# Optimization experiments

Measured on AMD Instinct MI355X. Metric: run time of the kernel, lower is better.

The kernel has to match this reference:

```python
import jax, jax.numpy as jnp
import numpy as np

N_NODES = 100000
N_EDGES = 600000
IN_DIM = 128
OUT_DIM = 64


def setup_inputs() -> dict:
    key = jax.random.key(0)
    k1, k2, k3, k4, k5 = jax.random.split(key, 5)
    x = jax.random.normal(k1, (N_NODES, IN_DIM), dtype=jnp.float32)
    edge_index = jax.random.randint(k2, (2, N_EDGES), 0, N_NODES, dtype=jnp.int64)
    edge_weight = jax.random.uniform(k3, (N_EDGES,), dtype=jnp.float32)
    W1 = jax.random.normal(k4, (IN_DIM, IN_DIM), dtype=jnp.float32) / np.sqrt(IN_DIM)
    b1 = jnp.zeros((IN_DIM,), dtype=jnp.float32)
    W2 = jax.random.normal(k5, (IN_DIM, OUT_DIM), dtype=jnp.float32) / np.sqrt(IN_DIM)
    b2 = jnp.zeros((OUT_DIM,), dtype=jnp.float32)
    return {"x": x, "edge_index": edge_index, "edge_weight": edge_weight,
            "W1": W1, "b1": b1, "W2": W2, "b2": b2}


def _spmm(edge_index, edge_weight, h):
    # out[dst] = sum_{e: dst(e)=dst} w_e * h[src(e)]  -- normalized adjacency SpMM
    src, dst = edge_index[0], edge_index[1]
    msg = h[src] * edge_weight[:, None]          # [E, D] gather + scale
    return jax.ops.segment_sum(msg, dst, num_segments=h.shape[0])  # [N, D]


def reference(x, edge_index, edge_weight, W1, b1, W2, b2):
    # Layer 1: GCNConv(in,in) -> ReLU (dropout is identity in eval mode)
    h = _spmm(edge_index, edge_weight, x @ W1) + b1
    h = jax.nn.relu(h)
    # Layer 2: GCNConv(in,out)
    out = _spmm(edge_index, edge_weight, h @ W2) + b2
    return out
```

## Files before the change

kernel.cpp:

```cpp
#include <hip/hip_runtime.h>

#define NN 100000
#define NE 600000
#define DIN 128
#define DOUT 64
#define SCAN_B 512
#define NBLK ((NN + SCAN_B - 1) / SCAN_B)
#define HIST_B ((NE + 255) / 256)
#define G1_BM 128
#define G1B ((NN + G1_BM - 1) / G1_BM)
#define ZB ((NN + 255) / 256)
#define W1B (DIN * DIN / 256)
#define W2B (DIN * DOUT / 256)
#define XS_PITCH 136
#define RP_PITCH 144

typedef __attribute__((ext_vector_type(8))) short bf16x8;
typedef __attribute__((ext_vector_type(4))) short s16x4;
typedef __attribute__((ext_vector_type(4))) float f32x4;
typedef __attribute__((ext_vector_type(2))) float f32x2;

__device__ inline short f2bf(float f) {
  union { float f; unsigned u; } v; v.f = f;
  unsigned r = (v.u + 0x7FFF + ((v.u >> 16) & 1)) >> 16;
  return (short)r;
}
__device__ inline float bf2f(unsigned short u) {
  union { unsigned u; float f; } v; v.u = ((unsigned)u) << 16;
  return v.f;
}
__device__ inline unsigned char f2fp8(float f) {
  unsigned pk = __builtin_amdgcn_cvt_pk_fp8_f32(f, f, 0, false);
  return (unsigned char)(pk & 0xff);
}
__device__ inline void fma_fp8x16(uint4 q, float w, float* acc) {
  f32x2 f;
  f = __builtin_amdgcn_cvt_pk_f32_fp8(q.x, false); acc[0] += w * f[0];  acc[1] += w * f[1];
  f = __builtin_amdgcn_cvt_pk_f32_fp8(q.x, true);  acc[2] += w * f[0];  acc[3] += w * f[1];
  f = __builtin_amdgcn_cvt_pk_f32_fp8(q.y, false); acc[4] += w * f[0];  acc[5] += w * f[1];
  f = __builtin_amdgcn_cvt_pk_f32_fp8(q.y, true);  acc[6] += w * f[0];  acc[7] += w * f[1];
  f = __builtin_amdgcn_cvt_pk_f32_fp8(q.z, false); acc[8] += w * f[0];  acc[9] += w * f[1];
  f = __builtin_amdgcn_cvt_pk_f32_fp8(q.z, true);  acc[10] += w * f[0]; acc[11] += w * f[1];
  f = __builtin_amdgcn_cvt_pk_f32_fp8(q.w, false); acc[12] += w * f[0]; acc[13] += w * f[1];
  f = __builtin_amdgcn_cvt_pk_f32_fp8(q.w, true);  acc[14] += w * f[0]; acc[15] += w * f[1];
}

__global__ __launch_bounds__(256) void prep_kernel(int* __restrict__ cnt,
                                                   const float* __restrict__ W1,
                                                   short* __restrict__ w1t,
                                                   const float* __restrict__ W2,
                                                   short* __restrict__ w2t) {
  const int b = blockIdx.x, t = threadIdx.x;
  if (b < ZB) {
    int i = b * 256 + t;
    if (i < NN) cnt[i] = 0;
  } else if (b < ZB + W1B) {
    int i = (b - ZB) * 256 + t;
    int n = i >> 7, k = i & 127;
    w1t[i] = f2bf(W1[k * DIN + n]);
  } else {
    int i = (b - ZB - W1B) * 256 + t;
    int n = i >> 7, k = i & 127;
    w2t[i] = f2bf(W2[k * DOUT + n]);
  }
}

__global__ __launch_bounds__(256) void hist_kernel(const int* __restrict__ ei,
                                                   int* __restrict__ cnt,
                                                   int* __restrict__ rank) {
  int e = blockIdx.x * 256 + threadIdx.x;
  if (e < NE) rank[e] = atomicAdd(&cnt[ei[NE + e]], 1);
}

__global__ __launch_bounds__(512) void scan_local_kernel(const int* __restrict__ cnt,
                                                         int* __restrict__ row_ptr,
                                                         int* __restrict__ blk_sum) {
  __shared__ int s[512];
  const int b = blockIdx.x, t = threadIdx.x;
  const int i = b * 512 + t;
  int v = (i < NN) ? cnt[i] : 0;
  s[t] = v;
  __syncthreads();
  for (int off = 1; off < 512; off <<= 1) {
    int u = (t >= off) ? s[t - off] : 0;
    __syncthreads();
    s[t] += u;
    __syncthreads();
  }
  if (i < NN) row_ptr[i] = s[t] - v;
  if (t == 511) blk_sum[b] = s[511];
}

__global__ __launch_bounds__(512) void scan_add_kernel(int* __restrict__ row_ptr,
                                                       const int* __restrict__ blk_sum) {
  __shared__ int s[512];
  const int b = blockIdx.x, t = threadIdx.x;
  s[t] = (t < NBLK) ? blk_sum[t] : 0;
  __syncthreads();
  for (int off = 1; off < 512; off <<= 1) {
    int u = (t >= off) ? s[t - off] : 0;
    __syncthreads();
    s[t] += u;
    __syncthreads();
  }
  int off = (b > 0) ? s[b - 1] : 0;
  const int i = b * 512 + t;
  if (i < NN) row_ptr[i] += off;
  if (b == 0 && t == 0) row_ptr[NN] = NE;
}

__global__ __launch_bounds__(256) void scatter_kernel(const int* __restrict__ ei,
                                                      const float* __restrict__ ew,
                                                      const int* __restrict__ row_ptr,
                                                      const int* __restrict__ rank,
                                                      int2* __restrict__ ep) {
  int e = blockIdx.x * 256 + threadIdx.x;
  if (e >= NE) return;
  int src = ei[e];
  int dst = ei[NE + e];
  int pos = row_ptr[dst] + rank[e];
  ep[pos] = make_int2(src, __float_as_int(ew[e]));
}

__global__ __launch_bounds__(256) void gemm1_kernel(const float* __restrict__ x,
                                                    const short* __restrict__ w1t,
                                                    unsigned char* __restrict__ h0) {
  __shared__ short xs[G1_BM][XS_PITCH];
  const int t = threadIdx.x;
  const int row0 = blockIdx.x * G1_BM;
#pragma unroll
  for (int i = 0; i < 16; ++i) {
    int f = t + i * 256;
    int r = f >> 5, c4 = f & 31;
    int gr = row0 + r;
    float4 v = (gr < NN) ? *(const float4*)&x[(size_t)gr * DIN + c4 * 4]
                         : make_float4(0.f, 0.f, 0.f, 0.f);
    s16x4 s;
    s.x = f2bf(v.x); s.y = f2bf(v.y); s.z = f2bf(v.z); s.w = f2bf(v.w);
    *(s16x4*)&xs[r][c4 * 4] = s;
  }
  __syncthreads();

  const int wave = t >> 6, lane = t & 63;
  const int nlane = lane & 15, quad = lane >> 4;
  const int mbase = wave * 32;
  f32x4 acc[2][8];
#pragma unroll
  for (int mt = 0; mt < 2; ++mt)
#pragma unroll
    for (int nt = 0; nt < 8; ++nt) acc[mt][nt] = (f32x4){0.f, 0.f, 0.f, 0.f};

#pragma unroll
  for (int ks = 0; ks < 4; ++ks) {
    const int koff = ks * 32 + quad * 8;
    bf16x8 a0 = *(const bf16x8*)&xs[mbase + nlane][koff];
    bf16x8 a1 = *(const bf16x8*)&xs[mbase + 16 + nlane][koff];
#pragma unroll
    for (int nt = 0; nt < 8; ++nt) {
      bf16x8 b = *(const bf16x8*)&w1t[(size_t)(nt * 16 + nlane) * DIN + koff];
      acc[0][nt] = __builtin_amdgcn_mfma_f32_16x16x32_bf16(a0, b, acc[0][nt], 0, 0, 0);
      acc[1][nt] = __builtin_amdgcn_mfma_f32_16x16x32_bf16(a1, b, acc[1][nt], 0, 0, 0);
    }
  }

  __syncthreads();
  unsigned char* lsb = (unsigned char*)xs;
#pragma unroll
  for (int mt = 0; mt < 2; ++mt)
#pragma unroll
    for (int nt = 0; nt < 8; ++nt)
#pragma unroll
      for (int rg = 0; rg < 4; ++rg)
        lsb[(mbase + mt * 16 + quad * 4 + rg) * RP_PITCH + nt * 16 + nlane] =
            f2fp8(acc[mt][nt][rg]);
  __syncthreads();
  {
    const int r = t >> 1, half = t & 1;
    const int gr = row0 + r;
    if (gr < NN) {
      const uint4* s = (const uint4*)(lsb + r * RP_PITCH + half * 64);
      uint4* d = (uint4*)&h0[(size_t)gr * DIN + half * 64];
      d[0] = s[0]; d[1] = s[1]; d[2] = s[2]; d[3] = s[3];
    }
  }
}

__global__ __launch_bounds__(512) void spmm1_gemm2_kernel(const int* __restrict__ rp,
                                                          const int2* __restrict__ ep,
                                                          const unsigned char* __restrict__ h,
                                                          const float* __restrict__ b1,
                                                          const short* __restrict__ w2t,
                                                          short* __restrict__ h2) {
  __shared__ short xs[G1_BM][XS_PITCH];
  const int t = threadIdx.x;
  const int row0 = blockIdx.x * G1_BM;
  const int sub = t >> 3, lane8 = t & 7;
  float bb[16];
  *(float4*)&bb[0]  = *(const float4*)&b1[lane8 * 16];
  *(float4*)&bb[4]  = *(const float4*)&b1[lane8 * 16 + 4];
  *(float4*)&bb[8]  = *(const float4*)&b1[lane8 * 16 + 8];
  *(float4*)&bb[12] = *(const float4*)&b1[lane8 * 16 + 12];

#pragma unroll
  for (int batch = 0; batch < 2; ++batch) {
    const int r = batch * 64 + sub;
    const int row = row0 + r;
    float acc[16];
#pragma unroll
    for (int j = 0; j < 16; ++j) acc[j] = 0.f;
    if (row < NN) {
      const int b0 = rp[row], e1 = rp[row + 1];
      int i = b0;
      for (; i + 4 <= e1; i += 4) {
        int2 p0 = ep[i], p1 = ep[i + 1], p2 = ep[i + 2], p3 = ep[i + 3];
        uint4 q0 = *(const uint4*)&h[(size_t)p0.x * DIN + lane8 * 16];
        uint4 q1 = *(const uint4*)&h[(size_t)p1.x * DIN + lane8 * 16];
        uint4 q2 = *(const uint4*)&h[(size_t)p2.x * DIN + lane8 * 16];
        uint4 q3 = *(const uint4*)&h[(size_t)p3.x * DIN + lane8 * 16];
        fma_fp8x16(q0, __int_as_float(p0.y), acc);
        fma_fp8x16(q1, __int_as_float(p1.y), acc);
        fma_fp8x16(q2, __int_as_float(p2.y), acc);
        fma_fp8x16(q3, __int_as_float(p3.y), acc);
      }
      if (i + 2 <= e1) {
        int2 p0 = ep[i], p1 = ep[i + 1];
        uint4 q0 = *(const uint4*)&h[(size_t)p0.x * DIN + lane8 * 16];
        uint4 q1 = *(const uint4*)&h[(size_t)p1.x * DIN + lane8 * 16];
        fma_fp8x16(q0, __int_as_float(p0.y), acc);
        fma_fp8x16(q1, __int_as_float(p1.y), acc);
        i += 2;
      }
      if (i < e1) {
        int2 p0 = ep[i];
        uint4 q0 = *(const uint4*)&h[(size_t)p0.x * DIN + lane8 * 16];
        fma_fp8x16(q0, __int_as_float(p0.y), acc);
      }
    }
    bf16x8 o0, o1;
#pragma unroll
    for (int j = 0; j < 8; ++j) {
      o0[j] = f2bf(fmaxf(acc[j] + bb[j], 0.f));
      o1[j] = f2bf(fmaxf(acc[8 + j] + bb[8 + j], 0.f));
    }
    *(bf16x8*)&xs[r][lane8 * 16] = o0;
    *(bf16x8*)&xs[r][lane8 * 16 + 8] = o1;
  }
  __syncthreads();

  const int wave = t >> 6, lane = t & 63;
  const int nlane = lane & 15, quad = lane >> 4;
  const int mbase = wave * 16;
  f32x4 acc2[4];
#pragma unroll
  for (int nt = 0; nt < 4; ++nt) acc2[nt] = (f32x4){0.f, 0.f, 0.f, 0.f};
#pragma unroll
  for (int ks = 0; ks < 4; ++ks) {
    const int koff = ks * 32 + quad * 8;
    bf16x8 a0 = *(const bf16x8*)&xs[mbase + nlane][koff];
#pragma unroll
    for (int nt = 0; nt < 4; ++nt) {
      bf16x8 bfr = *(const bf16x8*)&w2t[(size_t)(nt * 16 + nlane) * DIN + koff];
      acc2[nt] = __builtin_amdgcn_mfma_f32_16x16x32_bf16(a0, bfr, acc2[nt], 0, 0, 0);
    }
  }

  __syncthreads();
  unsigned char* lsb = (unsigned char*)xs;
#pragma unroll
  for (int nt = 0; nt < 4; ++nt)
#pragma unroll
    for (int rg = 0; rg < 4; ++rg)
      *(short*)(lsb + (mbase + quad * 4 + rg) * RP_PITCH + (nt * 16 + nlane) * 2) =
          f2bf(acc2[nt][rg]);
  __syncthreads();
  {
    const int r = t >> 2, q = t & 3;
    const int gr = row0 + r;
    if (gr < NN) {
      const uint4* s = (const uint4*)(lsb + r * RP_PITCH + q * 32);
      uint4* d = (uint4*)&h2[(size_t)gr * DOUT + q * 16];
      d[0] = s[0]; d[1] = s[1];
    }
  }
}

__global__ __launch_bounds__(256) void spmm2_kernel(const int* __restrict__ rp,
                                                    const int2* __restrict__ ep,
                                                    const short* __restrict__ h,
                                                    const float* __restrict__ bias,
                                                    float* __restrict__ out) {
  const int row = blockIdx.x * 32 + (threadIdx.x >> 3);
  const int lane = threadIdx.x & 7;
  if (row >= NN) return;
  const int b = rp[row], e = rp[row + 1];
  float acc[8];
#pragma unroll
  for (int j = 0; j < 8; ++j) acc[j] = 0.f;
  int i = b;
  for (; i + 4 <= e; i += 4) {
    int2 p0 = ep[i], p1 = ep[i + 1], p2 = ep[i + 2], p3 = ep[i + 3];
    bf16x8 v0 = *(const bf16x8*)&h[(size_t)p0.x * DOUT + lane * 8];
    bf16x8 v1 = *(const bf16x8*)&h[(size_t)p1.x * DOUT + lane * 8];
    bf16x8 v2 = *(const bf16x8*)&h[(size_t)p2.x * DOUT + lane * 8];
    bf16x8 v3 = *(const bf16x8*)&h[(size_t)p3.x * DOUT + lane * 8];
    float w0 = __int_as_float(p0.y), w1 = __int_as_float(p1.y);
    float w2 = __int_as_float(p2.y), w3 = __int_as_float(p3.y);
#pragma unroll
    for (int j = 0; j < 8; ++j)
      acc[j] += w0 * bf2f((unsigned short)v0[j]) + w1 * bf2f((unsigned short)v1[j]) +
                w2 * bf2f((unsigned short)v2[j]) + w3 * bf2f((unsigned short)v3[j]);
  }
  if (i + 2 <= e) {
    int2 p0 = ep[i], p1 = ep[i + 1];
    bf16x8 v0 = *(const bf16x8*)&h[(size_t)p0.x * DOUT + lane * 8];
    bf16x8 v1 = *(const bf16x8*)&h[(size_t)p1.x * DOUT + lane * 8];
    float w0 = __int_as_float(p0.y), w1 = __int_as_float(p1.y);
#pragma unroll
    for (int j = 0; j < 8; ++j)
      acc[j] += w0 * bf2f((unsigned short)v0[j]) + w1 * bf2f((unsigned short)v1[j]);
    i += 2;
  }
  if (i < e) {
    int2 p0 = ep[i];
    bf16x8 v0 = *(const bf16x8*)&h[(size_t)p0.x * DOUT + lane * 8];
    float w0 = __int_as_float(p0.y);
#pragma unroll
    for (int j = 0; j < 8; ++j) acc[j] += w0 * bf2f((unsigned short)v0[j]);
  }
#pragma unroll
  for (int j = 0; j < 8; ++j) acc[j] += bias[lane * 8 + j];
  *(float4*)&out[(size_t)row * DOUT + lane * 8] = make_float4(acc[0], acc[1], acc[2], acc[3]);
  *(float4*)&out[(size_t)row * DOUT + lane * 8 + 4] = make_float4(acc[4], acc[5], acc[6], acc[7]);
}

extern "C" void kernel_launch(void* const* d_in, const int* in_sizes, int n_in,
                              void* d_out, int out_size, void* d_ws, size_t ws_size,
                              hipStream_t stream) {
  const float* x  = (const float*)d_in[0];
  const int*   ei = (const int*)d_in[1];
  const float* ew = (const float*)d_in[2];
  const float* W1 = (const float*)d_in[3];
  const float* b1 = (const float*)d_in[4];
  const float* W2 = (const float*)d_in[5];
  const float* b2 = (const float*)d_in[6];
  float* out = (float*)d_out;

  char* p = (char*)d_ws;
  int*   cnt     = (int*)p;                 p += sizeof(int) * NN;
  int*   row_ptr = (int*)p;                 p += sizeof(int) * (NN + 4);
  int*   blk_sum = (int*)p;                 p += sizeof(int) * (NBLK + 4);
  int*   rank    = (int*)p;                 p += sizeof(int) * NE;
  int2*  ep      = (int2*)p;                p += sizeof(int2) * NE;
  short* w1t     = (short*)p;               p += sizeof(short) * DIN * DIN;
  short* w2t     = (short*)p;               p += sizeof(short) * DIN * DOUT;
  unsigned char* h0 = (unsigned char*)p;    p += (size_t)NN * DIN;
  short* h2      = (short*)p;

  prep_kernel<<<ZB + W1B + W2B, 256, 0, stream>>>(cnt, W1, w1t, W2, w2t);
  hist_kernel<<<HIST_B, 256, 0, stream>>>(ei, cnt, rank);
  scan_local_kernel<<<NBLK, 512, 0, stream>>>(cnt, row_ptr, blk_sum);
  scan_add_kernel<<<NBLK, 512, 0, stream>>>(row_ptr, blk_sum);
  scatter_kernel<<<HIST_B, 256, 0, stream>>>(ei, ew, row_ptr, rank, ep);
  gemm1_kernel<<<G1B, 256, 0, stream>>>(x, w1t, h0);
  spmm1_gemm2_kernel<<<G1B, 512, 0, stream>>>(row_ptr, ep, h0, b1, w2t, h2);
  spmm2_kernel<<<(NN + 31) / 32, 256, 0, stream>>>(row_ptr, ep, h2, b2, out);
}
```

Baseline: 231.5 us.

## Stage gathered neighbor rows into LDS via async global_load_lds in both SpMMs

Both SpMM kernels now process 64-row tiles and first gather every neighbor feature row of the tile into shared memory with direct global-to-LDS 16-byte loads. The chunk index is XOR-swizzled to avoid bank conflicts, and edge weights are staged in LDS alongside. Per-row accumulation then reads from LDS, with a fallback global path when a tile has more edges than the buffer capacity. This aims to issue all gathers at once for more memory-level parallelism and to hide gather latency. The cost is heavy LDS use (about 57KB), which limits occupancy, plus an extra barrier.

```diff
diff --git a/kernel.cpp b/kernel.cpp
--- a/kernel.cpp
+++ b/kernel.cpp
@@ -9,6 +9,10 @@
 #define HIST_B ((NE + 255) / 256)
 #define G1_BM 128
 #define G1B ((NN + G1_BM - 1) / G1_BM)
+#define SP_BM 64
+#define SPB ((NN + SP_BM - 1) / SP_BM)
+#define E_CAP 448
+#define NIT 14
 #define ZB ((NN + 255) / 256)
 #define W1B (DIN * DIN / 256)
 #define W2B (DIN * DOUT / 256)
@@ -32,6 +36,11 @@
 __device__ inline unsigned char f2fp8(float f) {
   unsigned pk = __builtin_amdgcn_cvt_pk_fp8_f32(f, f, 0, false);
   return (unsigned char)(pk & 0xff);
+}
+__device__ __forceinline__ void gl16(const void* g, void* l) {
+  __builtin_amdgcn_global_load_lds(
+      (const __attribute__((address_space(1))) void*)g,
+      (__attribute__((address_space(3))) void*)l, 16, 0, 0);
 }
 __device__ inline void fma_fp8x16(uint4 q, float w, float* acc) {
   f32x2 f;
@@ -43,6 +52,13 @@
   f = __builtin_amdgcn_cvt_pk_f32_fp8(q.z, true);  acc[10] += w * f[0]; acc[11] += w * f[1];
   f = __builtin_amdgcn_cvt_pk_f32_fp8(q.w, false); acc[12] += w * f[0]; acc[13] += w * f[1];
   f = __builtin_amdgcn_cvt_pk_f32_fp8(q.w, true);  acc[14] += w * f[0]; acc[15] += w * f[1];
+}
+__device__ inline void fma_bf16x8(uint4 q, float w, float* acc) {
+  unsigned u;
+  u = q.x; acc[0] += w * __uint_as_float(u << 16); acc[1] += w * __uint_as_float(u & 0xffff0000u);
+  u = q.y; acc[2] += w * __uint_as_float(u << 16); acc[3] += w * __uint_as_float(u & 0xffff0000u);
+  u = q.z; acc[4] += w * __uint_as_float(u << 16); acc[5] += w * __uint_as_float(u & 0xffff0000u);
+  u = q.w; acc[6] += w * __uint_as_float(u << 16); acc[7] += w * __uint_as_float(u & 0xffff0000u);
 }
 
 __global__ __launch_bounds__(256) void prep_kernel(int* __restrict__ cnt,
@@ -185,69 +201,83 @@
   }
 }
 
-__global__ __launch_bounds__(512) void spmm1_gemm2_kernel(const int* __restrict__ rp,
+__global__ __launch_bounds__(256) void spmm1_gemm2_kernel(const int* __restrict__ rp,
                                                           const int2* __restrict__ ep,
                                                           const unsigned char* __restrict__ h,
                                                           const float* __restrict__ b1,
                                                           const short* __restrict__ w2t,
                                                           short* __restrict__ h2) {
-  __shared__ short xs[G1_BM][XS_PITCH];
+  __shared__ int rpl[SP_BM + 4];
+  __shared__ float ws[E_CAP];
+  __shared__ uint4 gbuf[E_CAP * 8];
+  __shared__ short xs[SP_BM][XS_PITCH];
   const int t = threadIdx.x;
-  const int row0 = blockIdx.x * G1_BM;
-  const int sub = t >> 3, lane8 = t & 7;
-  float bb[16];
-  *(float4*)&bb[0]  = *(const float4*)&b1[lane8 * 16];
-  *(float4*)&bb[4]  = *(const float4*)&b1[lane8 * 16 + 4];
-  *(float4*)&bb[8]  = *(const float4*)&b1[lane8 * 16 + 8];
-  *(float4*)&bb[12] = *(const float4*)&b1[lane8 * 16 + 12];
-
-#pragma unroll
-  for (int batch = 0; batch < 2; ++batch) {
-    const int r = batch * 64 + sub;
-    const int row = row0 + r;
-    float acc[16];
-#pragma unroll
-    for (int j = 0; j < 16; ++j) acc[j] = 0.f;
-    if (row < NN) {
-      const int b0 = rp[row], e1 = rp[row + 1];
-      int i = b0;
-      for (; i + 4 <= e1; i += 4) {
-        int2 p0 = ep[i], p1 = ep[i + 1], p2 = ep[i + 2], p3 = ep[i + 3];
-        uint4 q0 = *(const uint4*)&h[(size_t)p0.x * DIN + lane8 * 16];
-        uint4 q1 = *(const uint4*)&h[(size_t)p1.x * DIN + lane8 * 16];
-        uint4 q2 = *(const uint4*)&h[(size_t)p2.x * DIN + lane8 * 16];
-        uint4 q3 = *(const uint4*)&h[(size_t)p3.x * DIN + lane8 * 16];
-        fma_fp8x16(q0, __int_as_float(p0.y), acc);
-        fma_fp8x16(q1, __int_as_float(p1.y), acc);
-        fma_fp8x16(q2, __int_as_float(p2.y), acc);
-        fma_fp8x16(q3, __int_as_float(p3.y), acc);
-      }
-      if (i + 2 <= e1) {
-        int2 p0 = ep[i], p1 = ep[i + 1];
-        uint4 q0 = *(const uint4*)&h[(size_t)p0.x * DIN + lane8 * 16];
-        uint4 q1 = *(const uint4*)&h[(size_t)p1.x * DIN + lane8 * 16];
-        fma_fp8x16(q0, __int_as_float(p0.y), acc);
-        fma_fp8x16(q1, __int_as_float(p1.y), acc);
-        i += 2;
-      }
-      if (i < e1) {
-        int2 p0 = ep[i];
-        uint4 q0 = *(const uint4*)&h[(size_t)p0.x * DIN + lane8 * 16];
-        fma_fp8x16(q0, __int_as_float(p0.y), acc);
-      }
-    }
-    bf16x8 o0, o1;
-#pragma unroll
-    for (int j = 0; j < 8; ++j) {
-      o0[j] = f2bf(fmaxf(acc[j] + bb[j], 0.f));
-      o1[j] = f2bf(fmaxf(acc[8 + j] + bb[8 + j], 0.f));
-    }
-    *(bf16x8*)&xs[r][lane8 * 16] = o0;
-    *(bf16x8*)&xs[r][lane8 * 16 + 8] = o1;
-  }
-  __syncthreads();
-
+  const int row0 = blockIdx.x * SP_BM;
+  if (t <= SP_BM) rpl[t] = rp[min(row0 + t, NN)];
+  __syncthreads();
+  const int e0 = rpl[0];
+  const int ne = rpl[SP_BM] - e0;
+  const int ncap = min(ne, E_CAP);
+  const int ncap8 = ncap * 8;
   const int wave = t >> 6, lane = t & 63;
+
+  int2 evs[NIT];
+#pragma unroll
+  for (int i = 0; i < NIT; ++i) {
+    int c = wave * 64 + i * 256 + lane;
+    evs[i] = (c < ncap8) ? ep[e0 + (c >> 3)] : make_int2(0, 0);
+  }
+#pragma unroll
+  for (int i = 0; i < NIT; ++i) {
+    int cb = wave * 64 + i * 256;
+    int c = cb + lane;
+    if (c < ncap8) {
+      int le = c >> 3;
+      if ((c & 7) == 0) ws[le] = __int_as_float(evs[i].y);
+      int j = (c & 7) ^ (le & 7);
+      gl16(h + (size_t)evs[i].x * DIN + j * 16, (void*)&gbuf[cb]);
+    }
+  }
+  __syncthreads();
+
+  const int r = t >> 2, lane4 = t & 3;
+  const int ea = rpl[r] - e0, eb = rpl[r + 1] - e0;
+  float acc[32];
+#pragma unroll
+  for (int j2 = 0; j2 < 32; ++j2) acc[j2] = 0.f;
+  int le = ea;
+  for (; le < eb && le < ncap; ++le) {
+    float w = ws[le];
+    int s = le & 7;
+    uint4 qlo = gbuf[le * 8 + ((2 * lane4) ^ s)];
+    uint4 qhi = gbuf[le * 8 + ((2 * lane4 + 1) ^ s)];
+    fma_fp8x16(qlo, w, acc);
+    fma_fp8x16(qhi, w, acc + 16);
+  }
+  for (; le < eb; ++le) {
+    int2 ev = ep[e0 + le];
+    float w = __int_as_float(ev.y);
+    const uint4* q = (const uint4*)&h[(size_t)ev.x * DIN + lane4 * 32];
+    uint4 qlo = q[0], qhi = q[1];
+    fma_fp8x16(qlo, w, acc);
+    fma_fp8x16(qhi, w, acc + 16);
+  }
+  {
+    float bb[32];
+#pragma unroll
+    for (int j2 = 0; j2 < 8; ++j2)
+      *(float4*)&bb[j2 * 4] = *(const float4*)&b1[lane4 * 32 + j2 * 4];
+#pragma unroll
+    for (int g = 0; g < 4; ++g) {
+      bf16x8 o;
+#pragma unroll
+      for (int j2 = 0; j2 < 8; ++j2)
+        o[j2] = f2bf(fmaxf(acc[g * 8 + j2] + bb[g * 8 + j2], 0.f));
+      *(bf16x8*)&xs[r][lane4 * 32 + g * 8] = o;
+    }
+  }
+  __syncthreads();
+
   const int nlane = lane & 15, quad = lane >> 4;
   const int mbase = wave * 16;
   f32x4 acc2[4];
@@ -274,11 +304,11 @@
           f2bf(acc2[nt][rg]);
   __syncthreads();
   {
-    const int r = t >> 2, q = t & 3;
-    const int gr = row0 + r;
+    const int r2 = t >> 2, q2 = t & 3;
+    const int gr = row0 + r2;
     if (gr < NN) {
-      const uint4* s = (const uint4*)(lsb + r * RP_PITCH + q * 32);
-      uint4* d = (uint4*)&h2[(size_t)gr * DOUT + q * 16];
+      const uint4* s = (const uint4*)(lsb + r2 * RP_PITCH + q2 * 32);
+      uint4* d = (uint4*)&h2[(size_t)gr * DOUT + q2 * 16];
       d[0] = s[0]; d[1] = s[1];
     }
   }
@@ -289,48 +319,75 @@
                                                     const short* __restrict__ h,
                                                     const float* __restrict__ bias,
                                                     float* __restrict__ out) {
-  const int row = blockIdx.x * 32 + (threadIdx.x >> 3);
-  const int lane = threadIdx.x & 7;
-  if (row >= NN) return;
-  const int b = rp[row], e = rp[row + 1];
-  float acc[8];
-#pragma unroll
-  for (int j = 0; j < 8; ++j) acc[j] = 0.f;
-  int i = b;
-  for (; i + 4 <= e; i += 4) {
-    int2 p0 = ep[i], p1 = ep[i + 1], p2 = ep[i + 2], p3 = ep[i + 3];
-    bf16x8 v0 = *(const bf16x8*)&h[(size_t)p0.x * DOUT + lane * 8];
-    bf16x8 v1 = *(const bf16x8*)&h[(size_t)p1.x * DOUT + lane * 8];
-    bf16x8 v2 = *(const bf16x8*)&h[(size_t)p2.x * DOUT + lane * 8];
-    bf16x8 v3 = *(const bf16x8*)&h[(size_t)p3.x * DOUT + lane * 8];
-    float w0 = __int_as_float(p0.y), w1 = __int_as_float(p1.y);
-    float w2 = __int_as_float(p2.y), w3 = __int_as_float(p3.y);
-#pragma unroll
-    for (int j = 0; j < 8; ++j)
-      acc[j] += w0 * bf2f((unsigned short)v0[j]) + w1 * bf2f((unsigned short)v1[j]) +
-                w2 * bf2f((unsigned short)v2[j]) + w3 * bf2f((unsigned short)v3[j]);
-  }
-  if (i + 2 <= e) {
-    int2 p0 = ep[i], p1 = ep[i + 1];
-    bf16x8 v0 = *(const bf16x8*)&h[(size_t)p0.x * DOUT + lane * 8];
-    bf16x8 v1 = *(const bf16x8*)&h[(size_t)p1.x * DOUT + lane * 8];
-    float w0 = __int_as_float(p0.y), w1 = __int_as_float(p1.y);
-#pragma unroll
-    for (int j = 0; j < 8; ++j)
-      acc[j] += w0 * bf2f((unsigned short)v0[j]) + w1 * bf2f((unsigned short)v1[j]);
-    i += 2;
-  }
-  if (i < e) {
-    int2 p0 = ep[i];
-    bf16x8 v0 = *(const bf16x8*)&h[(size_t)p0.x * DOUT + lane * 8];
-    float w0 = __int_as_float(p0.y);
-#pragma unroll
-    for (int j = 0; j < 8; ++j) acc[j] += w0 * bf2f((unsigned short)v0[j]);
-  }
-#pragma unroll
-  for (int j = 0; j < 8; ++j) acc[j] += bias[lane * 8 + j];
-  *(float4*)&out[(size_t)row * DOUT + lane * 8] = make_float4(acc[0], acc[1], acc[2], acc[3]);
-  *(float4*)&out[(size_t)row * DOUT + lane * 8 + 4] = make_float4(acc[4], acc[5], acc[6], acc[7]);
+  __shared__ int rpl[SP_BM + 4];
+  __shared__ float ws[E_CAP];
+  __shared__ uint4 gbuf[E_CAP * 8];
+  const int t = threadIdx.x;
+  const int row0 = blockIdx.x * SP_BM;
+  if (t <= SP_BM) rpl[t] = rp[min(row0 + t, NN)];
+  __syncthreads();
+  const int e0 = rpl[0];
+  const int ne = rpl[SP_BM] - e0;
+  const int ncap = min(ne, E_CAP);
+  const int ncap8 = ncap * 8;
+  const int wave = t >> 6, lane = t & 63;
+  const unsigned char* hb = (const unsigned char*)h;
+
+  int2 evs[NIT];
+#pragma unroll
+  for (int i = 0; i < NIT; ++i) {
+    int c = wave * 64 + i * 256 + lane;
+    evs[i] = (c < ncap8) ? ep[e0 + (c >> 3)] : make_int2(0, 0);
+  }
+#pragma unroll
+  for (int i = 0; i < NIT; ++i) {
+    int cb = wave * 64 + i * 256;
+    int c = cb + lane;
+    if (c < ncap8) {
+      int le = c >> 3;
+      if ((c & 7) == 0) ws[le] = __int_as_float(evs[i].y);
+      int j = (c & 7) ^ (le & 7);
+      gl16(hb + (size_t)evs[i].x * 128 + j * 16, (void*)&gbuf[cb]);
+    }
+  }
+  __syncthreads();
+
+  const int r = t >> 2, lane4 = t & 3;
+  const int row = row0 + r;
+  const int ea = rpl[r] - e0, eb = rpl[r + 1] - e0;
+  float acc[16];
+#pragma unroll
+  for (int j2 = 0; j2 < 16; ++j2) acc[j2] = 0.f;
+  int le = ea;
+  for (; le < eb && le < ncap; ++le) {
+    float w = ws[le];
+    int s = le & 7;
+    uint4 qlo = gbuf[le * 8 + ((2 * lane4) ^ s)];
+    uint4 qhi = gbuf[le * 8 + ((2 * lane4 + 1) ^ s)];
+    fma_bf16x8(qlo, w, acc);
+    fma_bf16x8(qhi, w, acc + 8);
+  }
+  for (; le < eb; ++le) {
+    int2 ev = ep[e0 + le];
+    float w = __int_as_float(ev.y);
+    const uint4* q = (const uint4*)&hb[(size_t)ev.x * 128 + lane4 * 32];
+    uint4 qlo = q[0], qhi = q[1];
+    fma_bf16x8(qlo, w, acc);
+    fma_bf16x8(qhi, w, acc + 8);
+  }
+  if (row < NN) {
+    float bb[16];
+#pragma unroll
+    for (int j2 = 0; j2 < 4; ++j2)
+      *(float4*)&bb[j2 * 4] = *(const float4*)&bias[lane4 * 16 + j2 * 4];
+#pragma unroll
+    for (int j2 = 0; j2 < 16; ++j2) acc[j2] += bb[j2];
+    float* op = &out[(size_t)row * DOUT + lane4 * 16];
+#pragma unroll
+    for (int j2 = 0; j2 < 4; ++j2)
+      *(float4*)&op[j2 * 4] =
+          make_float4(acc[j2 * 4], acc[j2 * 4 + 1], acc[j2 * 4 + 2], acc[j2 * 4 + 3]);
+  }
 }
 
 extern "C" void kernel_launch(void* const* d_in, const int* in_sizes, int n_in,
@@ -362,6 +419,6 @@
   scan_add_kernel<<<NBLK, 512, 0, stream>>>(row_ptr, blk_sum);
   scatter_kernel<<<HIST_B, 256, 0, stream>>>(ei, ew, row_ptr, rank, ep);
   gemm1_kernel<<<G1B, 256, 0, stream>>>(x, w1t, h0);
-  spmm1_gemm2_kernel<<<G1B, 512, 0, stream>>>(row_ptr, ep, h0, b1, w2t, h2);
-  spmm2_kernel<<<(NN + 31) / 32, 256, 0, stream>>>(row_ptr, ep, h2, b2, out);
-}
+  spmm1_gemm2_kernel<<<SPB, 256, 0, stream>>>(row_ptr, ep, h0, b1, w2t, h2);
+  spmm2_kernel<<<SPB, 256, 0, stream>>>(row_ptr, ep, h2, b2, out);
+}
```

Measured after the change: 258.0 us. 1.11x slower.
